# Optimization experiments

Hardware: AMD Instinct MI355X
Metric: run time of the kernel (lower is better)

Reference implementation:

```python
import jax, jax.numpy as jnp
import numpy as np


def setup_inputs() -> dict:
    key = jax.random.key(0)
    k1, k2 = jax.random.split(key)
    N, M, D = 16384, 16384, 3
    src_V = jax.random.normal(k1, (N, D), dtype=jnp.float32)
    tar_V = jax.random.normal(k2, (M, D), dtype=jnp.float32)
    return {"src_V": src_V, "tar_V": tar_V}


def reference(src_V, tar_V):
    # 1-NN: for each target point find nearest source point (replaces cKDTree).
    # Squared distances via ||t||^2 - 2 t.s + ||s||^2 ; [M, N]
    d2 = (
        jnp.sum(tar_V * tar_V, axis=1, keepdims=True)
        - 2.0 * (tar_V @ src_V.T)
        + jnp.sum(src_V * src_V, axis=1)[None, :]
    )
    ii = jnp.argmin(d2, axis=1)            # [M] nearest src index per target
    diff = src_V[ii] - tar_V               # [M, 3]
    loss = 0.5 * jnp.sum(diff * diff)
    return loss
```

## Files before the change

kernel.cpp:

```cpp
#include <hip/hip_runtime.h>
#include <math.h>

constexpr int N_SRC = 16384;
constexpr int M_TAR = 16384;

constexpr int BLOCKS = 512;
constexpr int TPB = 512;
constexpr int CHUNKS = 256;
constexpr int TILE = 2048;
constexpr int TILES = N_SRC / TILE;
constexpr int ROWS_PT = TILE / CHUNKS;
constexpr int IPT = ROWS_PT / 2;
constexpr int TPT = 16;
constexpr int PPT = TILE / TPB;
constexpr int NROWS = N_SRC / CHUNKS;

__global__ void zero_out(float* __restrict__ out) {
    if (threadIdx.x == 0) out[0] = 0.0f;
}

__device__ __forceinline__ void min3(float& b, float e0, float e1) {
    asm("v_min3_f32 %0, %0, %1, %2"
        : "+v"(b) : "v"(e0), "v"(e1));
}

__device__ __forceinline__ float to_sgpr(float x) {
    return __uint_as_float(
        (unsigned)__builtin_amdgcn_readfirstlane((int)__float_as_uint(x)));
}

__global__
__attribute__((amdgpu_flat_work_group_size(TPB, TPB)))
__attribute__((amdgpu_waves_per_eu(4, 4)))
void nn11(const float* __restrict__ src,
          const float* __restrict__ tar,
          float* __restrict__ out) {
    __shared__ float4 tile[2 * TILE];

    const int tid   = threadIdx.x;
    const int g     = tid >> 8;
    const int chunk = tid & 255;
    const int tbase = blockIdx.x * 32;

    float txm2[TPT], tym2[TPT], tzm2[TPT], best[TPT];
#pragma unroll
    for (int k = 0; k < TPT; ++k) {
        int T = tbase + g * TPT + k;
        txm2[k] = to_sgpr(-2.0f * tar[3 * T + 0]);
        tym2[k] = to_sgpr(-2.0f * tar[3 * T + 1]);
        tzm2[k] = to_sgpr(-2.0f * tar[3 * T + 2]);
        best[k] = INFINITY;
    }

#pragma unroll
    for (int r = 0; r < PPT; ++r) {
        int p = tid + r * TPB;
        const float* q = src + 3 * p;
        float x = q[0], y = q[1], z = q[2];
        tile[p] = make_float4(x, y, z, fmaf(x, x, fmaf(y, y, z * z)));
    }
    __syncthreads();

    auto compute = [&](int cb) {
#pragma unroll
        for (int i = 0; i < IPT; ++i) {
            float4 s0 = tile[cb + (2 * i + 0) * CHUNKS + chunk];
            float4 s1 = tile[cb + (2 * i + 1) * CHUNKS + chunk];
#pragma unroll
            for (int k = 0; k < TPT; ++k) {
                float t0 = fmaf(s0.z, tzm2[k], s0.w);
                t0 = fmaf(s0.y, tym2[k], t0);
                t0 = fmaf(s0.x, txm2[k], t0);
                float t1 = fmaf(s1.z, tzm2[k], s1.w);
                t1 = fmaf(s1.y, tym2[k], t1);
                t1 = fmaf(s1.x, txm2[k], t1);
                min3(best[k], t0, t1);
            }
        }
    };

#pragma unroll 1
    for (int tl = 0; tl < TILES - 1; ++tl) {
        float px[PPT], py[PPT], pz[PPT];
#pragma unroll
        for (int r = 0; r < PPT; ++r) {
            const float* q = src + 3 * ((tl + 1) * TILE + tid + r * TPB);
            px[r] = q[0]; py[r] = q[1]; pz[r] = q[2];
        }
        __builtin_amdgcn_sched_barrier(0);

        compute((tl & 1) * TILE);

        const int wb = ((tl + 1) & 1) * TILE;
#pragma unroll
        for (int r = 0; r < PPT; ++r) {
            float x = px[r], y = py[r], z = pz[r];
            tile[wb + tid + r * TPB] =
                make_float4(x, y, z, fmaf(x, x, fmaf(y, y, z * z)));
        }
        __syncthreads();
    }
    compute(((TILES - 1) & 1) * TILE);

    __syncthreads();
    float* fv = (float*)tile;
#pragma unroll
    for (int k = 0; k < TPT; ++k) {
        fv[(g * TPT + k) * CHUNKS + chunk] = best[k];
    }
    __syncthreads();

    const int tprime = tid >> 4;
    const int sub    = tid & 15;
    float bv = fv[tprime * CHUNKS + sub];
    int   bc = sub;
#pragma unroll
    for (int m = 1; m < CHUNKS / 16; ++m) {
        float v = fv[tprime * CHUNKS + sub + 16 * m];
        if (v < bv) { bv = v; bc = sub + 16 * m; }
    }
#pragma unroll
    for (int s = 8; s >= 1; s >>= 1) {
        float vv = __shfl_xor(bv, s, 64);
        int   cc = __shfl_xor(bc, s, 64);
        if (vv < bv) { bv = vv; bc = cc; }
    }

    const int T = tbase + tprime;
    const float tx = tar[3 * T + 0], ty = tar[3 * T + 1], tz = tar[3 * T + 2];
    const float rxm2 = -2.0f * tx, rym2 = -2.0f * ty, rzm2 = -2.0f * tz;
    int myrow = NROWS;
#pragma unroll
    for (int rr = 0; rr < NROWS / 16; ++rr) {
        int r = sub + 16 * rr;
        int j = r * CHUNKS + bc;
        const float* q = src + 3 * j;
        float x = q[0], y = q[1], z = q[2];
        float w = fmaf(x, x, fmaf(y, y, z * z));
        float v = fmaf(z, rzm2, w);
        v = fmaf(y, rym2, v);
        v = fmaf(x, rxm2, v);
        if (v == bv && r < myrow) myrow = r;
    }
#pragma unroll
    for (int s = 8; s >= 1; s >>= 1) {
        int r2 = __shfl_xor(myrow, s, 64);
        if (r2 < myrow) myrow = r2;
    }
    __syncthreads();

    if (sub == 0) {
        int j = myrow * CHUNKS + bc;
        float dx = src[3 * j + 0] - tx;
        float dy = src[3 * j + 1] - ty;
        float dz = src[3 * j + 2] - tz;
        fv[tprime] = 0.5f * fmaf(dx, dx, fmaf(dy, dy, dz * dz));
    }
    __syncthreads();
    if (tid == 0) {
        float ssum = 0.0f;
#pragma unroll
        for (int i = 0; i < 32; ++i) ssum += fv[i];
        atomicAdd(out, ssum);
    }
}

extern "C" void kernel_launch(void* const* d_in, const int* in_sizes, int n_in,
                              void* d_out, int out_size, void* d_ws, size_t ws_size,
                              hipStream_t stream) {
    const float* src = (const float*)d_in[0];
    const float* tar = (const float*)d_in[1];
    float* out = (float*)d_out;
    (void)d_ws; (void)ws_size;

    zero_out<<<1, 64, 0, stream>>>(out);
    nn11<<<BLOCKS, TPB, 0, stream>>>(src, tar, out);
}
```

Before: 85.14 us.

## Double threads per block with smaller tiles for higher wave occupancy

Raises the block to 1024 threads, splitting the source points across 512 chunks with a 1024-point tile, and targets 8 waves per EU instead of 4. Each thread now handles two source points per tile against 16 targets. This shortens the per-thread inner loop and the tie-break scan, and relies on more resident waves to hide LDS and global latency. In exchange there are twice as many tile iterations and barriers, a larger LDS allocation, and a tighter register budget at 8 waves per EU, which could cause spilling.

```diff
diff --git a/kernel.cpp b/kernel.cpp
--- a/kernel.cpp
+++ b/kernel.cpp
@@ -5,14 +5,11 @@
 constexpr int M_TAR = 16384;
 
 constexpr int BLOCKS = 512;
-constexpr int TPB = 512;
-constexpr int CHUNKS = 256;
-constexpr int TILE = 2048;
+constexpr int TPB = 1024;
+constexpr int CHUNKS = 512;
+constexpr int TILE = 1024;
 constexpr int TILES = N_SRC / TILE;
-constexpr int ROWS_PT = TILE / CHUNKS;
-constexpr int IPT = ROWS_PT / 2;
 constexpr int TPT = 16;
-constexpr int PPT = TILE / TPB;
 constexpr int NROWS = N_SRC / CHUNKS;
 
 __global__ void zero_out(float* __restrict__ out) {
@@ -31,15 +28,15 @@
 
 __global__
 __attribute__((amdgpu_flat_work_group_size(TPB, TPB)))
-__attribute__((amdgpu_waves_per_eu(4, 4)))
-void nn11(const float* __restrict__ src,
+__attribute__((amdgpu_waves_per_eu(8, 8)))
+void nn12(const float* __restrict__ src,
           const float* __restrict__ tar,
           float* __restrict__ out) {
-    __shared__ float4 tile[2 * TILE];
+    __shared__ float4 lds[4 * TILE];
 
     const int tid   = threadIdx.x;
-    const int g     = tid >> 8;
-    const int chunk = tid & 255;
+    const int g     = tid >> 9;
+    const int chunk = tid & 511;
     const int tbase = blockIdx.x * 32;
 
     float txm2[TPT], tym2[TPT], tzm2[TPT], best[TPT];
@@ -52,75 +49,62 @@
         best[k] = INFINITY;
     }
 
-#pragma unroll
-    for (int r = 0; r < PPT; ++r) {
-        int p = tid + r * TPB;
-        const float* q = src + 3 * p;
+    {
+        const float* q = src + 3 * tid;
         float x = q[0], y = q[1], z = q[2];
-        tile[p] = make_float4(x, y, z, fmaf(x, x, fmaf(y, y, z * z)));
+        lds[tid] = make_float4(x, y, z, fmaf(x, x, fmaf(y, y, z * z)));
     }
     __syncthreads();
 
     auto compute = [&](int cb) {
+        float4 s0 = lds[cb + chunk];
+        float4 s1 = lds[cb + CHUNKS + chunk];
 #pragma unroll
-        for (int i = 0; i < IPT; ++i) {
-            float4 s0 = tile[cb + (2 * i + 0) * CHUNKS + chunk];
-            float4 s1 = tile[cb + (2 * i + 1) * CHUNKS + chunk];
-#pragma unroll
-            for (int k = 0; k < TPT; ++k) {
-                float t0 = fmaf(s0.z, tzm2[k], s0.w);
-                t0 = fmaf(s0.y, tym2[k], t0);
-                t0 = fmaf(s0.x, txm2[k], t0);
-                float t1 = fmaf(s1.z, tzm2[k], s1.w);
-                t1 = fmaf(s1.y, tym2[k], t1);
-                t1 = fmaf(s1.x, txm2[k], t1);
-                min3(best[k], t0, t1);
-            }
+        for (int k = 0; k < TPT; ++k) {
+            float t0 = fmaf(s0.z, tzm2[k], s0.w);
+            t0 = fmaf(s0.y, tym2[k], t0);
+            t0 = fmaf(s0.x, txm2[k], t0);
+            float t1 = fmaf(s1.z, tzm2[k], s1.w);
+            t1 = fmaf(s1.y, tym2[k], t1);
+            t1 = fmaf(s1.x, txm2[k], t1);
+            min3(best[k], t0, t1);
         }
     };
 
 #pragma unroll 1
     for (int tl = 0; tl < TILES - 1; ++tl) {
-        float px[PPT], py[PPT], pz[PPT];
-#pragma unroll
-        for (int r = 0; r < PPT; ++r) {
-            const float* q = src + 3 * ((tl + 1) * TILE + tid + r * TPB);
-            px[r] = q[0]; py[r] = q[1]; pz[r] = q[2];
-        }
+        const float* q = src + 3 * ((tl + 1) * TILE + tid);
+        float px = q[0], py = q[1], pz = q[2];
         __builtin_amdgcn_sched_barrier(0);
 
         compute((tl & 1) * TILE);
 
         const int wb = ((tl + 1) & 1) * TILE;
-#pragma unroll
-        for (int r = 0; r < PPT; ++r) {
-            float x = px[r], y = py[r], z = pz[r];
-            tile[wb + tid + r * TPB] =
-                make_float4(x, y, z, fmaf(x, x, fmaf(y, y, z * z)));
-        }
+        lds[wb + tid] = make_float4(px, py, pz,
+                                    fmaf(px, px, fmaf(py, py, pz * pz)));
         __syncthreads();
     }
     compute(((TILES - 1) & 1) * TILE);
 
     __syncthreads();
-    float* fv = (float*)tile;
+    float* fv = (float*)lds;
 #pragma unroll
     for (int k = 0; k < TPT; ++k) {
         fv[(g * TPT + k) * CHUNKS + chunk] = best[k];
     }
     __syncthreads();
 
-    const int tprime = tid >> 4;
-    const int sub    = tid & 15;
+    const int tprime = tid >> 5;
+    const int sub    = tid & 31;
     float bv = fv[tprime * CHUNKS + sub];
     int   bc = sub;
 #pragma unroll
-    for (int m = 1; m < CHUNKS / 16; ++m) {
-        float v = fv[tprime * CHUNKS + sub + 16 * m];
-        if (v < bv) { bv = v; bc = sub + 16 * m; }
+    for (int m = 1; m < CHUNKS / 32; ++m) {
+        float v = fv[tprime * CHUNKS + sub + 32 * m];
+        if (v < bv) { bv = v; bc = sub + 32 * m; }
     }
 #pragma unroll
-    for (int s = 8; s >= 1; s >>= 1) {
+    for (int s = 16; s >= 1; s >>= 1) {
         float vv = __shfl_xor(bv, s, 64);
         int   cc = __shfl_xor(bc, s, 64);
         if (vv < bv) { bv = vv; bc = cc; }
@@ -129,21 +113,19 @@
     const int T = tbase + tprime;
     const float tx = tar[3 * T + 0], ty = tar[3 * T + 1], tz = tar[3 * T + 2];
     const float rxm2 = -2.0f * tx, rym2 = -2.0f * ty, rzm2 = -2.0f * tz;
-    int myrow = NROWS;
-#pragma unroll
-    for (int rr = 0; rr < NROWS / 16; ++rr) {
-        int r = sub + 16 * rr;
-        int j = r * CHUNKS + bc;
+    int myrow;
+    {
+        int j = sub * CHUNKS + bc;
         const float* q = src + 3 * j;
         float x = q[0], y = q[1], z = q[2];
         float w = fmaf(x, x, fmaf(y, y, z * z));
         float v = fmaf(z, rzm2, w);
         v = fmaf(y, rym2, v);
         v = fmaf(x, rxm2, v);
-        if (v == bv && r < myrow) myrow = r;
+        myrow = (v == bv) ? sub : NROWS;
     }
 #pragma unroll
-    for (int s = 8; s >= 1; s >>= 1) {
+    for (int s = 16; s >= 1; s >>= 1) {
         int r2 = __shfl_xor(myrow, s, 64);
         if (r2 < myrow) myrow = r2;
     }
@@ -174,5 +156,5 @@
     (void)d_ws; (void)ws_size;
 
     zero_out<<<1, 64, 0, stream>>>(out);
-    nn11<<<BLOCKS, TPB, 0, stream>>>(src, tar, out);
+    nn12<<<BLOCKS, TPB, 0, stream>>>(src, tar, out);
 }
```

Measured after the change: 129.3 us. +51.9%, slower.

## Precompute packed float4 sources in a prep kernel and stream them directly from global

Applied to the files above, without the earlier changes.

A prep kernel now packs each source point with its squared norm into a float4 workspace and also zeroes the output. The main kernel drops the double-buffered LDS tile and its barriers, and instead has each thread load its float4 pairs straight from global (L2-cached), software-pipelined one step ahead. This removes per-block recomputation of norms, the LDS staging and the sync overhead. In exchange it adds a kernel launch, relies on L2 bandwidth for repeated source reads across 512 blocks, and changes the occupancy hints to launch_bounds(512,2).

```diff
diff --git a/kernel.cpp b/kernel.cpp
--- a/kernel.cpp
+++ b/kernel.cpp
@@ -7,16 +7,17 @@
 constexpr int BLOCKS = 512;
 constexpr int TPB = 512;
 constexpr int CHUNKS = 256;
-constexpr int TILE = 2048;
-constexpr int TILES = N_SRC / TILE;
-constexpr int ROWS_PT = TILE / CHUNKS;
-constexpr int IPT = ROWS_PT / 2;
 constexpr int TPT = 16;
-constexpr int PPT = TILE / TPB;
 constexpr int NROWS = N_SRC / CHUNKS;
 
-__global__ void zero_out(float* __restrict__ out) {
-    if (threadIdx.x == 0) out[0] = 0.0f;
+__global__ void prep(const float* __restrict__ src,
+                     float4* __restrict__ ws,
+                     float* __restrict__ out) {
+    int i = blockIdx.x * blockDim.x + threadIdx.x;
+    if (i == 0) out[0] = 0.0f;
+    const float* q = src + 3 * i;
+    float x = q[0], y = q[1], z = q[2];
+    ws[i] = make_float4(x, y, z, fmaf(x, x, fmaf(y, y, z * z)));
 }
 
 __device__ __forceinline__ void min3(float& b, float e0, float e1) {
@@ -29,13 +30,12 @@
         (unsigned)__builtin_amdgcn_readfirstlane((int)__float_as_uint(x)));
 }
 
-__global__
-__attribute__((amdgpu_flat_work_group_size(TPB, TPB)))
-__attribute__((amdgpu_waves_per_eu(4, 4)))
-void nn11(const float* __restrict__ src,
+__global__ __launch_bounds__(TPB, 2)
+void nn14(const float4* __restrict__ ws,
+          const float* __restrict__ src,
           const float* __restrict__ tar,
           float* __restrict__ out) {
-    __shared__ float4 tile[2 * TILE];
+    __shared__ float fv[32 * CHUNKS];
 
     const int tid   = threadIdx.x;
     const int g     = tid >> 8;
@@ -52,58 +52,31 @@
         best[k] = INFINITY;
     }
 
+    auto comp = [&](float4 s0, float4 s1) {
 #pragma unroll
-    for (int r = 0; r < PPT; ++r) {
-        int p = tid + r * TPB;
-        const float* q = src + 3 * p;
-        float x = q[0], y = q[1], z = q[2];
-        tile[p] = make_float4(x, y, z, fmaf(x, x, fmaf(y, y, z * z)));
-    }
-    __syncthreads();
-
-    auto compute = [&](int cb) {
-#pragma unroll
-        for (int i = 0; i < IPT; ++i) {
-            float4 s0 = tile[cb + (2 * i + 0) * CHUNKS + chunk];
-            float4 s1 = tile[cb + (2 * i + 1) * CHUNKS + chunk];
-#pragma unroll
-            for (int k = 0; k < TPT; ++k) {
-                float t0 = fmaf(s0.z, tzm2[k], s0.w);
-                t0 = fmaf(s0.y, tym2[k], t0);
-                t0 = fmaf(s0.x, txm2[k], t0);
-                float t1 = fmaf(s1.z, tzm2[k], s1.w);
-                t1 = fmaf(s1.y, tym2[k], t1);
-                t1 = fmaf(s1.x, txm2[k], t1);
-                min3(best[k], t0, t1);
-            }
+        for (int k = 0; k < TPT; ++k) {
+            float t0 = fmaf(s0.z, tzm2[k], s0.w);
+            t0 = fmaf(s0.y, tym2[k], t0);
+            t0 = fmaf(s0.x, txm2[k], t0);
+            float t1 = fmaf(s1.z, tzm2[k], s1.w);
+            t1 = fmaf(s1.y, tym2[k], t1);
+            t1 = fmaf(s1.x, txm2[k], t1);
+            min3(best[k], t0, t1);
         }
     };
 
+    float4 s0 = ws[0 * CHUNKS + chunk];
+    float4 s1 = ws[1 * CHUNKS + chunk];
 #pragma unroll 1
-    for (int tl = 0; tl < TILES - 1; ++tl) {
-        float px[PPT], py[PPT], pz[PPT];
-#pragma unroll
-        for (int r = 0; r < PPT; ++r) {
-            const float* q = src + 3 * ((tl + 1) * TILE + tid + r * TPB);
-            px[r] = q[0]; py[r] = q[1]; pz[r] = q[2];
-        }
+    for (int r = 0; r + 2 < NROWS; r += 2) {
+        float4 n0 = ws[(r + 2) * CHUNKS + chunk];
+        float4 n1 = ws[(r + 3) * CHUNKS + chunk];
         __builtin_amdgcn_sched_barrier(0);
+        comp(s0, s1);
+        s0 = n0; s1 = n1;
+    }
+    comp(s0, s1);
 
-        compute((tl & 1) * TILE);
-
-        const int wb = ((tl + 1) & 1) * TILE;
-#pragma unroll
-        for (int r = 0; r < PPT; ++r) {
-            float x = px[r], y = py[r], z = pz[r];
-            tile[wb + tid + r * TPB] =
-                make_float4(x, y, z, fmaf(x, x, fmaf(y, y, z * z)));
-        }
-        __syncthreads();
-    }
-    compute(((TILES - 1) & 1) * TILE);
-
-    __syncthreads();
-    float* fv = (float*)tile;
 #pragma unroll
     for (int k = 0; k < TPT; ++k) {
         fv[(g * TPT + k) * CHUNKS + chunk] = best[k];
@@ -171,8 +144,9 @@
     const float* src = (const float*)d_in[0];
     const float* tar = (const float*)d_in[1];
     float* out = (float*)d_out;
-    (void)d_ws; (void)ws_size;
+    float4* ws = (float4*)d_ws;
+    (void)ws_size;
 
-    zero_out<<<1, 64, 0, stream>>>(out);
-    nn11<<<BLOCKS, TPB, 0, stream>>>(src, tar, out);
+    prep<<<N_SRC / 512, 512, 0, stream>>>(src, ws, out);
+    nn14<<<BLOCKS, TPB, 0, stream>>>(ws, src, tar, out);
 }
```

Result: no change. 85.07 us (-0.1%).
